# Performance work log

Hardware: AMD Instinct MI355X
Metric: run time of the kernel (lower is better)

Reference implementation:

```python
import jax, jax.numpy as jnp
import numpy as np

D_MODEL = 1024
NUM_HEADS = 16
D_HEAD = D_MODEL // NUM_HEADS  # 64, used only as softmax scale
DFF = 4096
EPS = 1e-6


def _layernorm(x, gamma, beta):
    mu = jnp.mean(x, axis=-1, keepdims=True)
    var = jnp.mean(jnp.square(x - mu), axis=-1, keepdims=True)
    return (x - mu) * jax.lax.rsqrt(var + EPS) * gamma + beta


def _mha(q_in, kv, score, Wq, bq, Wk, bk, Wv, bv, Wo, bo):
    # q_in: [B,Sq,d]; kv: [Sv,d] (broadcast over batch, mirroring unsqueeze(0))
    Q = q_in @ Wq.T + bq                      # [B,Sq,d]
    K = kv @ Wk.T + bk                        # [Sv,d]
    V = kv @ Wv.T + bv                        # [Sv,d]
    scores = (jnp.einsum('bqd,kd->bqk', Q, K) + score) / jnp.sqrt(
        jnp.asarray(D_HEAD, dtype=jnp.float32))
    w = jax.nn.softmax(scores, axis=-1)       # [B,Sq,Sv]
    out = jnp.einsum('bqk,kd->bqd', w, V)     # [B,Sq,d]
    return out @ Wo.T + bo


def setup_inputs() -> dict:
    key = jax.random.key(0)
    ks = jax.random.split(key, 20)
    B, Sq, Sv = 4, 2048, 196
    s = 0.02
    inp = {
        'text_tensor': jax.random.normal(ks[0], (B, Sq, D_MODEL), jnp.float32),
        'visual_tensor': jax.random.normal(ks[1], (Sv, D_MODEL), jnp.float32),
        'score_matrix': jax.random.normal(ks[2], (B, Sq, Sv), jnp.float32),
        'text_tensor2': jax.random.normal(ks[3], (B, Sq, D_MODEL), jnp.float32),
        'visual_tensor2': jax.random.normal(ks[4], (Sv, D_MODEL), jnp.float32),
        'score_matrix2': jax.random.normal(ks[5], (B, Sq, Sv), jnp.float32),
        'Wq': jax.random.normal(ks[6], (D_MODEL, D_MODEL), jnp.float32) * s,
        'bq': jnp.zeros((D_MODEL,), jnp.float32),
        'Wk': jax.random.normal(ks[7], (D_MODEL, D_MODEL), jnp.float32) * s,
        'bk': jnp.zeros((D_MODEL,), jnp.float32),
        'Wv': jax.random.normal(ks[8], (D_MODEL, D_MODEL), jnp.float32) * s,
        'bv': jnp.zeros((D_MODEL,), jnp.float32),
        'Wo': jax.random.normal(ks[9], (D_MODEL, D_MODEL), jnp.float32) * s,
        'bo': jnp.zeros((D_MODEL,), jnp.float32),
        'W1': jax.random.normal(ks[10], (DFF, D_MODEL), jnp.float32) * s,
        'b1': jnp.zeros((DFF,), jnp.float32),
        'W2': jax.random.normal(ks[11], (D_MODEL, DFF), jnp.float32) * s,
        'b2': jnp.zeros((D_MODEL,), jnp.float32),
        'g1': jnp.ones((D_MODEL,), jnp.float32),
        'be1': jnp.zeros((D_MODEL,), jnp.float32),
        'g2': jnp.ones((D_MODEL,), jnp.float32),
        'be2': jnp.zeros((D_MODEL,), jnp.float32),
    }
    return inp


def reference(text_tensor, visual_tensor, score_matrix,
              text_tensor2, visual_tensor2, score_matrix2,
              Wq, bq, Wk, bk, Wv, bv, Wo, bo,
              W1, b1, W2, b2, g1, be1, g2, be2):
    # Branch 1 (dropout is identity in eval mode)
    a1 = _mha(text_tensor, visual_tensor, score_matrix,
              Wq, bq, Wk, bk, Wv, bv, Wo, bo)
    out1 = _layernorm(text_tensor + a1, g1, be1)
    # Branch 2 (shared attention weights, same layernorm1)
    a2 = _mha(text_tensor2, visual_tensor2, score_matrix2,
              Wq, bq, Wk, bk, Wv, bv, Wo, bo)
    out2 = _layernorm(text_tensor2 + a2, g1, be1)
    # Concat along features then MaxPool1d(kernel=2, stride=2) over last dim
    concat = jnp.concatenate([out1, out2], axis=2)       # [B,Sq,2d]
    B, Sq, _ = concat.shape
    pooled = jnp.max(concat.reshape(B, Sq, D_MODEL, 2), axis=-1)  # [B,Sq,d]
    # FFN + residual + layernorm2
    ffn = jax.nn.relu(pooled @ W1.T + b1) @ W2.T + b2
    return _layernorm(pooled + ffn, g2, be2)
```

## Files before the change

kernel.cpp:

```cpp
#include <hip/hip_runtime.h>
#include <hip/hip_bf16.h>
#include <cstdint>
#include <type_traits>

typedef unsigned short u16;
typedef __bf16 bf16x8 __attribute__((ext_vector_type(8)));
typedef float f32x4 __attribute__((ext_vector_type(4)));

#define LN_EPS 1e-6f

enum { BIAS_NONE = 0, BIAS_COL = 1, BIAS_ROW = 2, BIAS_COL2 = 3 };

__device__ __forceinline__ float b2f(u16 h) {
  union { unsigned u; float f; } v;
  v.u = ((unsigned)h) << 16;
  return v.f;
}
__device__ __forceinline__ u16 f2b(float x) {
  return __bfloat16_as_ushort(__float2bfloat16(x));
}

__device__ __forceinline__ void gld_lds16(const void* g, void* l) {
  __builtin_amdgcn_global_load_lds(
      (const __attribute__((address_space(1))) void*)g,
      (__attribute__((address_space(3))) void*)l, 16, 0, 0);
}

__device__ __forceinline__ void st8(float4 a, float4 b, u16* dst) {
  u16 t[8] = {f2b(a.x), f2b(a.y), f2b(a.z), f2b(a.w),
              f2b(b.x), f2b(b.y), f2b(b.z), f2b(b.w)};
  *reinterpret_cast<uint4*>(dst) = *reinterpret_cast<const uint4*>(t);
}

__device__ __forceinline__ void stage8_cvt(const float* src, size_t off,
                                           u16* dst) {
  const float* p = src + off;
  st8(*reinterpret_cast<const float4*>(p),
      *reinterpret_cast<const float4*>(p + 4), dst);
}

template <typename OutT, int BIAS, bool RELU, bool A_RAW, bool B_RAW, int TM,
          int TN, int BK, int NT, int LB>
__global__ __launch_bounds__(NT, LB) void gemm_db(
    const void* __restrict__ A, const void* __restrict__ A2,
    const void* __restrict__ B, const void* __restrict__ B2,
    const float* __restrict__ bias, const float* __restrict__ bias2,
    OutT* __restrict__ C, int M, int N, int K, int lda, int ldb, int MA,
    int NB, int ldc, int Msplit, int rowmask, int colsplit) {
  constexpr int SA = (TM * BK) / (NT * 8);
  constexpr int SB = (TN * BK) / (NT * 8);
  constexpr int AI = (NT == 512) ? 2 : ((TM == 128 && TN == 128) ? 4 : 2);
  constexpr int BJ = (TM == 64 && TN == 64) ? 2 : 4;
  __shared__ __align__(16) u16 As[2][TM * BK];
  __shared__ __align__(16) u16 Bs[2][TN * BK];
  const int tid = threadIdx.x;
  const int lane = tid & 63;
  const int wv = tid >> 6;
  int wr, wc;
  if constexpr (NT == 512) {
    wr = (wv & 3) * 32; wc = (wv >> 2) * 64;
  } else if constexpr (TM == 128 && TN == 128) {
    wr = (wv >> 1) * 64; wc = (wv & 1) * 64;
  } else if constexpr (TM == 128 && TN == 64) {
    wr = wv * 32; wc = 0;
  } else {
    wr = (wv >> 1) * 32; wc = (wv & 1) * 32;
  }
  const int mrow = lane & 15;
  const int quad = lane >> 4;

  int bxi = blockIdx.x, byi = blockIdx.y;
  {
    const int gx = (int)gridDim.x;
    const int nwg = gx * (int)gridDim.y;
    if ((nwg & 7) == 0) {
      int wg = byi * gx + bxi;
      wg = (wg & 7) * (nwg >> 3) + (wg >> 3);
      bxi = wg % gx;
      byi = wg / gx;
    }
  }
  const int bm = byi * TM;
  const int bn = bxi * TN;

  f32x4 acc[AI][BJ];
#pragma unroll
  for (int i = 0; i < AI; i++)
#pragma unroll
    for (int j = 0; j < BJ; j++) acc[i][j] = f32x4{0.f, 0.f, 0.f, 0.f};

  const int e0 = tid * 8;
  const int r0t = e0 >> 5;
  const int swc8 = ((((e0 >> 3) & 3) ^ ((r0t >> 1) & 3)) << 3);

  const void* Asrc[SA];
  size_t aoff[SA];
#pragma unroll
  for (int s = 0; s < SA; s++) {
    const int h = (s * NT * 8) / (TM * 32);
    const int rb = ((s * NT * 8) % (TM * 32)) >> 5;
    int ra = bm + rb + r0t;
    if (ra >= MA) ra = MA - 1;
    Asrc[s] = (ra < Msplit) ? A : A2;
    const int rr = (ra < Msplit) ? ra : ra - Msplit;
    aoff[s] = (size_t)rr * lda + h * 32 + swc8;
  }
  const void* Bb = (bm < Msplit) ? B : B2;
  size_t boff[SB];
#pragma unroll
  for (int s = 0; s < SB; s++) {
    const int h = (s * NT * 8) / (TN * 32);
    const int rb = ((s * NT * 8) % (TN * 32)) >> 5;
    int rbn = bn + rb + r0t;
    if (rbn >= NB) rbn = NB - 1;
    boff[s] = (size_t)rbn * ldb + h * 32 + swc8;
  }

#pragma unroll
  for (int s = 0; s < SA; s++) {
    if constexpr (A_RAW) {
      const float* p = (const float*)Asrc[s] + aoff[s];
      st8(*reinterpret_cast<const float4*>(p),
          *reinterpret_cast<const float4*>(p + 4), &As[0][s * NT * 8 + e0]);
    } else {
      gld_lds16((const u16*)Asrc[s] + aoff[s], &As[0][s * NT * 8 + e0]);
    }
  }
#pragma unroll
  for (int s = 0; s < SB; s++) {
    if constexpr (B_RAW) {
      const float* p = (const float*)Bb + boff[s];
      st8(*reinterpret_cast<const float4*>(p),
          *reinterpret_cast<const float4*>(p + 4), &Bs[0][s * NT * 8 + e0]);
    } else {
      gld_lds16((const u16*)Bb + boff[s], &Bs[0][s * NT * 8 + e0]);
    }
  }
  __syncthreads();

  const int so = ((quad ^ ((mrow >> 1) & 3)) << 3);

  int cur = 0;
  for (int k0 = 0; k0 < K; k0 += BK) {
    const int nk = k0 + BK;
    const bool pf = nk < K;
    float4 fA[SA][2], fB[SB][2];
    if (pf) {
#pragma unroll
      for (int s = 0; s < SA; s++) {
        if constexpr (A_RAW) {
          const float* p = (const float*)Asrc[s] + aoff[s] + nk;
          fA[s][0] = *reinterpret_cast<const float4*>(p);
          fA[s][1] = *reinterpret_cast<const float4*>(p + 4);
        } else {
          gld_lds16((const u16*)Asrc[s] + aoff[s] + nk,
                    &As[cur ^ 1][s * NT * 8 + e0]);
        }
      }
#pragma unroll
      for (int s = 0; s < SB; s++) {
        if constexpr (B_RAW) {
          const float* p = (const float*)Bb + boff[s] + nk;
          fB[s][0] = *reinterpret_cast<const float4*>(p);
          fB[s][1] = *reinterpret_cast<const float4*>(p + 4);
        } else {
          gld_lds16((const u16*)Bb + boff[s] + nk,
                    &Bs[cur ^ 1][s * NT * 8 + e0]);
        }
      }
    }
#pragma unroll
    for (int h = 0; h < BK / 32; h++) {
      bf16x8 af[AI], bfm[BJ];
#pragma unroll
      for (int i = 0; i < AI; i++)
        af[i] = *reinterpret_cast<const bf16x8*>(
            &As[cur][h * TM * 32 + (wr + i * 16 + mrow) * 32 + so]);
#pragma unroll
      for (int j = 0; j < BJ; j++)
        bfm[j] = *reinterpret_cast<const bf16x8*>(
            &Bs[cur][h * TN * 32 + (wc + j * 16 + mrow) * 32 + so]);
#pragma unroll
      for (int i = 0; i < AI; i++)
#pragma unroll
        for (int j = 0; j < BJ; j++)
          acc[i][j] = __builtin_amdgcn_mfma_f32_16x16x32_bf16(
              af[i], bfm[j], acc[i][j], 0, 0, 0);
    }
    if (pf) {
      if constexpr (A_RAW) {
#pragma unroll
        for (int s = 0; s < SA; s++)
          st8(fA[s][0], fA[s][1], &As[cur ^ 1][s * NT * 8 + e0]);
      }
      if constexpr (B_RAW) {
#pragma unroll
        for (int s = 0; s < SB; s++)
          st8(fB[s][0], fB[s][1], &Bs[cur ^ 1][s * NT * 8 + e0]);
      }
    }
    __syncthreads();
    cur ^= 1;
  }

  const float* bp = (bm < Msplit) ? bias : bias2;
#pragma unroll
  for (int i = 0; i < AI; i++) {
#pragma unroll
    for (int j = 0; j < BJ; j++) {
#pragma unroll
      for (int r = 0; r < 4; r++) {
        const int gr = bm + wr + i * 16 + quad * 4 + r;
        const int gc = bn + wc + j * 16 + mrow;
        if (gr < M && gc < N) {
          float v = acc[i][j][r];
          if (BIAS == BIAS_COL) v += bp[gc];
          if (BIAS == BIAS_COL2)
            v += (gc < colsplit) ? bias[gc] : bias2[gc - colsplit];
          if (BIAS == BIAS_ROW) v += bp[gr & rowmask];
          if (RELU) v = fmaxf(v, 0.f);
          if constexpr (std::is_same<OutT, float>::value)
            C[(size_t)gr * ldc + gc] = v;
          else
            C[(size_t)gr * ldc + gc] = f2b(v);
        }
      }
    }
  }
}

__global__ __launch_bounds__(256) void cvt3_k(
    const float* __restrict__ s0, u16* __restrict__ d0,
    const float* __restrict__ s1, u16* __restrict__ d1,
    const float* __restrict__ s2, u16* __restrict__ d2, int blocksPer) {
  const int seg = blockIdx.x / blocksPer;
  const int b = blockIdx.x % blocksPer;
  const float* s = (seg == 0) ? s0 : ((seg == 1) ? s1 : s2);
  u16* d = (seg == 0) ? d0 : ((seg == 1) ? d1 : d2);
  const size_t i = ((size_t)b * 256 + threadIdx.x) * 8;
  stage8_cvt(s, i, d + i);
}

__global__ __launch_bounds__(256) void wqt_k(const float* __restrict__ src,
                                             u16* __restrict__ dst) {
  __shared__ float t[64][65];
  const int bx = blockIdx.x;
  const int by = blockIdx.y;
  const int tx = threadIdx.x & 63;
  const int ty = threadIdx.x >> 6;
#pragma unroll
  for (int i = 0; i < 16; i++)
    t[ty * 16 + i][tx] =
        src[(size_t)(by * 64 + ty * 16 + i) * 1024 + bx * 64 + tx];
  __syncthreads();
#pragma unroll
  for (int i = 0; i < 16; i++)
    dst[(size_t)(bx * 64 + ty * 16 + i) * 1024 + by * 64 + tx] =
        f2b(t[tx][ty * 16 + i]);
}

__global__ __launch_bounds__(256) void kb_k(const u16* __restrict__ Kc,
                                            const float* __restrict__ bq,
                                            float* __restrict__ kb, int ld) {
  const int wvi = blockIdx.x * 4 + (threadIdx.x >> 6);
  const int lane = threadIdx.x & 63;
  const int b = wvi / 224, s = wvi % 224;
  float sum = 0.f;
  if (s < 196) {
    const u16* row = Kc + (size_t)(b * 196 + s) * ld;
    for (int j = lane; j < 1024; j += 64) sum += b2f(row[j]) * bq[j];
  }
#pragma unroll
  for (int off = 32; off > 0; off >>= 1) sum += __shfl_xor(sum, off);
  if (lane == 0) kb[wvi] = sum;
}

__global__ __launch_bounds__(256) void softmax_k(
    u16* __restrict__ Sp, const float* __restrict__ sc1,
    const float* __restrict__ sc2) {
  const int row = blockIdx.x * 4 + (threadIdx.x >> 6);
  const int lane = threadIdx.x & 63;
  const float* score = (row < 8192) ? sc1 + (size_t)row * 196
                                    : sc2 + (size_t)(row - 8192) * 196;
  float x[4];
  float mx = -1e30f;
#pragma unroll
  for (int t = 0; t < 4; t++) {
    const int s = lane + 64 * t;
    float v = -1e30f;
    if (s < 196) v = (b2f(Sp[(size_t)row * 224 + s]) + score[s]) * 0.125f;
    x[t] = v;
    mx = fmaxf(mx, v);
  }
#pragma unroll
  for (int off = 32; off > 0; off >>= 1) mx = fmaxf(mx, __shfl_xor(mx, off));
  float sum = 0.f;
#pragma unroll
  for (int t = 0; t < 4; t++) {
    const int s = lane + 64 * t;
    const float e = (s < 196) ? expf(x[t] - mx) : 0.f;
    x[t] = e;
    sum += e;
  }
#pragma unroll
  for (int off = 32; off > 0; off >>= 1) sum += __shfl_xor(sum, off);
  const float inv = 1.f / sum;
#pragma unroll
  for (int t = 0; t < 4; t++) {
    const int s = lane + 64 * t;
    if (s < 224) Sp[(size_t)row * 224 + s] = f2b((s < 196) ? x[t] * inv : 0.f);
  }
}

__global__ __launch_bounds__(256) void ln_pool_k(
    const float* __restrict__ X1, const float* __restrict__ X2,
    const u16* __restrict__ Y, const float* __restrict__ g,
    const float* __restrict__ be, u16* __restrict__ pooled) {
  const int row16 = blockIdx.x;
  const int br = row16 >> 13;
  const int row = row16 & 8191;
  const int tid = threadIdx.x;
  const int lane = tid & 63;
  const int wv = tid >> 6;
  const float* X = (br ? X2 : X1) + (size_t)row * 1024;
  const u16* Yp = Y + (size_t)row16 * 1024;
  __shared__ float red[4];
  float v[4];
  float s = 0.f;
#pragma unroll
  for (int j = 0; j < 4; j++) {
    const float a = X[tid * 4 + j] + b2f(Yp[tid * 4 + j]);
    v[j] = a;
    s += a;
  }
#pragma unroll
  for (int off = 32; off > 0; off >>= 1) s += __shfl_xor(s, off);
  if (lane == 0) red[wv] = s;
  __syncthreads();
  const float mu = (red[0] + red[1] + red[2] + red[3]) * (1.f / 1024.f);
  __syncthreads();
  float var = 0.f;
#pragma unroll
  for (int j = 0; j < 4; j++) {
    const float d = v[j] - mu;
    var += d * d;
  }
#pragma unroll
  for (int off = 32; off > 0; off >>= 1) var += __shfl_xor(var, off);
  if (lane == 0) red[wv] = var;
  __syncthreads();
  var = (red[0] + red[1] + red[2] + red[3]) * (1.f / 1024.f);
  const float rs = rsqrtf(var + LN_EPS);
  float n[4];
#pragma unroll
  for (int j = 0; j < 4; j++)
    n[j] = (v[j] - mu) * rs * g[tid * 4 + j] + be[tid * 4 + j];
  const size_t pb = (size_t)row * 1024 + br * 512 + tid * 2;
  pooled[pb] = f2b(fmaxf(n[0], n[1]));
  pooled[pb + 1] = f2b(fmaxf(n[2], n[3]));
}

__global__ __launch_bounds__(256) void ln_out_k(
    const u16* __restrict__ X, const u16* __restrict__ Y,
    const float* __restrict__ g, const float* __restrict__ be,
    float* __restrict__ out) {
  const int row = blockIdx.x;
  const int tid = threadIdx.x;
  const int lane = tid & 63;
  const int wv = tid >> 6;
  __shared__ float red[4];
  float v[4];
  float s = 0.f;
  const size_t base = (size_t)row * 1024 + tid * 4;
#pragma unroll
  for (int j = 0; j < 4; j++) {
    const float a = b2f(X[base + j]) + b2f(Y[base + j]);
    v[j] = a;
    s += a;
  }
#pragma unroll
  for (int off = 32; off > 0; off >>= 1) s += __shfl_xor(s, off);
  if (lane == 0) red[wv] = s;
  __syncthreads();
  const float mu = (red[0] + red[1] + red[2] + red[3]) * (1.f / 1024.f);
  __syncthreads();
  float var = 0.f;
#pragma unroll
  for (int j = 0; j < 4; j++) {
    const float d = v[j] - mu;
    var += d * d;
  }
#pragma unroll
  for (int off = 32; off > 0; off >>= 1) var += __shfl_xor(var, off);
  if (lane == 0) red[wv] = var;
  __syncthreads();
  var = (red[0] + red[1] + red[2] + red[3]) * (1.f / 1024.f);
  const float rs = rsqrtf(var + LN_EPS);
#pragma unroll
  for (int j = 0; j < 4; j++)
    out[base + j] = (v[j] - mu) * rs * g[tid * 4 + j] + be[tid * 4 + j];
}

extern "C" void kernel_launch(void* const* d_in, const int* in_sizes, int n_in,
                              void* d_out, int out_size, void* d_ws,
                              size_t ws_size, hipStream_t stream) {
  const size_t MB = 1ull << 20;
  if (ws_size < 61 * MB) return;

  const float* text1 = (const float*)d_in[0];
  const float* vis1 = (const float*)d_in[1];
  const float* sc1 = (const float*)d_in[2];
  const float* text2 = (const float*)d_in[3];
  const float* vis2 = (const float*)d_in[4];
  const float* sc2 = (const float*)d_in[5];
  const float* Wq = (const float*)d_in[6];
  const float* bq = (const float*)d_in[7];
  const float* Wk = (const float*)d_in[8];
  const float* bk = (const float*)d_in[9];
  const float* Wv = (const float*)d_in[10];
  const float* bv = (const float*)d_in[11];
  const float* Wo = (const float*)d_in[12];
  const float* bo = (const float*)d_in[13];
  const float* W1 = (const float*)d_in[14];
  const float* b1 = (const float*)d_in[15];
  const float* W2 = (const float*)d_in[16];
  const float* b2 = (const float*)d_in[17];
  const float* g1 = (const float*)d_in[18];
  const float* be1 = (const float*)d_in[19];
  const float* g2 = (const float*)d_in[20];
  const float* be2 = (const float*)d_in[21];

  const int D = 1024, Sv = 196, SvP = 224, DFF = 4096;
  const int M2 = 16384;
  char* w = (char*)d_ws;
  u16* pooled = (u16*)(w + 0 * MB);
  u16* Wkb = (u16*)(w + 16 * MB);
  u16* Wvb = (u16*)(w + 18 * MB);
  u16* Wob = (u16*)(w + 20 * MB);
  u16* WqT = (u16*)(w + 22 * MB);
  u16* KVcat = (u16*)(w + 24 * MB);
  u16* K2cat = (u16*)(w + 26 * MB);
  u16* VWoT = (u16*)(w + 27 * MB);
  float* kb = (float*)(w + 28 * MB);
  u16* Spcat = (u16*)(w + 29 * MB);
  u16* Ocat = (u16*)d_out;
  u16* H = (u16*)(w + 16 * MB);
  u16* F = (u16*)(w + 48 * MB);
  u16* W1b = (u16*)((char*)d_out + 16 * MB);
  u16* W2b = (u16*)((char*)d_out + 24 * MB);

  auto grid = [](int m, int n, int tm, int tn) {
    return dim3((unsigned)((n + tn - 1) / tn), (unsigned)((m + tm - 1) / tm));
  };

  cvt3_k<<<dim3(3 * 512), 256, 0, stream>>>(Wk, Wkb, Wv, Wvb, Wo, Wob, 512);
  wqt_k<<<dim3(16, 16), 256, 0, stream>>>(Wq, WqT);

  gemm_db<u16, BIAS_COL2, false, true, false, 64, 64, 32, 256, 8>
      <<<grid(2 * Sv, 2 * D, 64, 64), 256, 0, stream>>>(
          vis1, vis2, Wkb, Wkb, bk, bv, KVcat, 2 * Sv, 2 * D, D, D, D, 2 * Sv,
          2 * D, 2 * D, Sv, 0, D);
  gemm_db<u16, BIAS_NONE, false, false, false, 64, 64, 32, 256, 8>
      <<<grid(2 * Sv, D, 64, 64), 256, 0, stream>>>(
          KVcat, KVcat, WqT, WqT, nullptr, nullptr, K2cat, 2 * Sv, D, D, 2 * D,
          D, 2 * Sv, D, D, 2 * Sv, 0, 0);
  kb_k<<<dim3(112), 256, 0, stream>>>(KVcat, bq, kb, 2 * D);
  gemm_db<u16, BIAS_COL, false, true, false, 64, 64, 32, 256, 8>
      <<<grid(M2, Sv, 64, 64), 256, 0, stream>>>(
          text1, text2, K2cat, K2cat + (size_t)Sv * D, kb, kb + SvP, Spcat, M2,
          Sv, D, D, D, M2, Sv, SvP, 8192, 0, 0);
  softmax_k<<<dim3(M2 / 4), 256, 0, stream>>>(Spcat, sc1, sc2);
  gemm_db<u16, BIAS_ROW, false, false, false, 64, 64, 32, 256, 8>
      <<<grid(2 * D, SvP, 64, 64), 256, 0, stream>>>(
          Wob, Wob, KVcat + D, KVcat + (size_t)Sv * 2 * D + D, bo, bo, VWoT,
          2 * D, SvP, D, D, 2 * D, 2 * D, Sv, SvP, D, D - 1, 0);
  gemm_db<u16, BIAS_NONE, false, false, false, 64, 64, 32, 256, 8>
      <<<grid(M2, D, 64, 64), 256, 0, stream>>>(
          Spcat, Spcat + (size_t)8192 * SvP, VWoT, VWoT + (size_t)D * SvP,
          nullptr, nullptr, Ocat, M2, D, SvP, SvP, SvP, M2, D, D, 8192, 0, 0);
  ln_pool_k<<<dim3(M2), 256, 0, stream>>>(text1, text2, Ocat, g1, be1, pooled);

  cvt3_k<<<dim3(2 * 2048), 256, 0, stream>>>(W1, W1b, W2, W2b, W2, W2b, 2048);

  for (int c = 0; c < 2; ++c) {
    const int r0 = c * 4096, rows = 4096;
    gemm_db<u16, BIAS_COL, true, false, false, 128, 128, 32, 256, 5>
        <<<grid(rows, DFF, 128, 128), 256, 0, stream>>>(
            pooled + (size_t)r0 * D, pooled + (size_t)r0 * D, W1b, W1b, b1, b1,
            H, rows, DFF, D, D, D, rows, DFF, DFF, rows, 0, 0);
    gemm_db<u16, BIAS_COL, false, false, false, 64, 64, 64, 256, 5>
        <<<grid(rows, D, 64, 64), 256, 0, stream>>>(
            H, H, W2b, W2b, b2, b2, F, rows, D, DFF, DFF, DFF, rows, D, D,
            rows, 0, 0);
    ln_out_k<<<dim3(rows), 256, 0, stream>>>(
        pooled + (size_t)r0 * D, F, g2, be2, (float*)d_out + (size_t)r0 * D);
  }
}
```

Before: 538.8 us.

## Add specialized 256x256 eight-wave pipelined GEMM for FFN up-projection

Replaces the generic 128x128 tiled GEMM for the first FFN layer (4096x4096x1024, bias+ReLU) with a hardcoded 256x256 tile kernel using 8 waves, split-K-half LDS buffers with XOR swizzle, direct global-to-LDS loads interleaved into eight phases per K pair, and setprio around MFMA bursts. Block indices are remapped for L2 locality. The larger tile raises arithmetic intensity and the finer-grained phase scheduling is meant to overlap loads with MFMA; the cost is heavy register and LDS use (occupancy 2 blocks) and a kernel hardwired to these exact dimensions.

```diff
diff --git a/kernel.cpp b/kernel.cpp
--- a/kernel.cpp
+++ b/kernel.cpp
@@ -37,6 +37,121 @@
   const float* p = src + off;
   st8(*reinterpret_cast<const float4*>(p),
       *reinterpret_cast<const float4*>(p + 4), dst);
+}
+
+#define PH8(BUF, KS, FH, VM, ...)                                           \
+  do {                                                                      \
+    asm volatile("s_waitcnt vmcnt(" #VM ")" ::: "memory");                  \
+    __builtin_amdgcn_sched_barrier(0);                                      \
+    __builtin_amdgcn_s_barrier();                                           \
+    __builtin_amdgcn_sched_barrier(0);                                      \
+    bf16x8 af[4], bfr[4];                                                   \
+    _Pragma("unroll") for (int j = 0; j < 4; j++) {                         \
+      const int ra = wm * 128 + ((FH) * 4 + j) * 16 + mrow;                 \
+      af[j] = *reinterpret_cast<const bf16x8*>(                             \
+          &As[BUF][KS][ra * 32 + ((quad ^ ((ra >> 1) & 3)) << 3)]);         \
+    }                                                                       \
+    _Pragma("unroll") for (int j = 0; j < 4; j++) {                         \
+      const int rb = wn * 64 + j * 16 + mrow;                               \
+      bfr[j] = *reinterpret_cast<const bf16x8*>(                            \
+          &Bs[BUF][KS][rb * 32 + ((quad ^ ((rb >> 1) & 3)) << 3)]);         \
+    }                                                                       \
+    __VA_ARGS__;                                                            \
+    __builtin_amdgcn_s_setprio(1);                                          \
+    _Pragma("unroll") for (int j = 0; j < 4; j++)                           \
+        _Pragma("unroll") for (int c = 0; c < 4; c++) acc[(FH) * 4 + j][c] = \
+            __builtin_amdgcn_mfma_f32_16x16x32_bf16(                        \
+                af[j], bfr[c], acc[(FH) * 4 + j][c], 0, 0, 0);              \
+    __builtin_amdgcn_s_setprio(0);                                          \
+  } while (0)
+
+__global__ __launch_bounds__(512, 2) void gemm_8p(
+    const u16* __restrict__ A, const u16* __restrict__ B,
+    const float* __restrict__ bias, u16* __restrict__ C) {
+  __shared__ __align__(16) u16 As[2][2][256 * 32];
+  __shared__ __align__(16) u16 Bs[2][2][256 * 32];
+  const int tid = threadIdx.x;
+  const int lane = tid & 63;
+  const int wid = tid >> 6;
+  const int wm = wid >> 2;
+  const int wn = wid & 3;
+  const int mrow = lane & 15;
+  const int quad = lane >> 4;
+  int bxi = blockIdx.x, byi = blockIdx.y;
+  {
+    int wg = byi * 16 + bxi;
+    wg = (wg & 7) * 32 + (wg >> 3);
+    bxi = wg & 15;
+    byi = wg >> 4;
+  }
+  const int bm = byi * 256;
+  const int bn = bxi * 256;
+
+  const int i0 = tid;
+  const int i1 = 512 + tid;
+  const int r0 = i0 >> 2, c0s = (((i0 & 3) ^ ((r0 >> 1) & 3)) << 3);
+  const int r1 = i1 >> 2, c1s = (((i1 & 3) ^ ((r1 >> 1) & 3)) << 3);
+  const size_t oa0 = (size_t)(bm + r0) * 1024 + c0s;
+  const size_t oa1 = (size_t)(bm + r1) * 1024 + c1s;
+  const size_t ob0 = (size_t)(bn + r0) * 1024 + c0s;
+  const size_t ob1 = (size_t)(bn + r1) * 1024 + c1s;
+
+#define STG_A(T, KH)                                                       \
+  do {                                                                     \
+    gld_lds16(A + oa0 + (T) * 64 + (KH) * 32, &As[(T) & 1][KH][i0 * 8]);   \
+    gld_lds16(A + oa1 + (T) * 64 + (KH) * 32, &As[(T) & 1][KH][i1 * 8]);   \
+  } while (0)
+#define STG_B(T, KH)                                                       \
+  do {                                                                     \
+    gld_lds16(B + ob0 + (T) * 64 + (KH) * 32, &Bs[(T) & 1][KH][i0 * 8]);   \
+    gld_lds16(B + ob1 + (T) * 64 + (KH) * 32, &Bs[(T) & 1][KH][i1 * 8]);   \
+  } while (0)
+
+  f32x4 acc[8][4];
+#pragma unroll
+  for (int i = 0; i < 8; i++)
+#pragma unroll
+    for (int j = 0; j < 4; j++) acc[i][j] = f32x4{0.f, 0.f, 0.f, 0.f};
+
+  STG_A(0, 0); STG_B(0, 0); STG_A(0, 1); STG_B(0, 1);
+  STG_A(1, 0); STG_B(1, 0);
+
+#pragma unroll 1
+  for (int t = 0; t < 14; t += 2) {
+    PH8(0, 0, 0, 8, STG_A(t + 1, 1));
+    PH8(0, 0, 1, 8, STG_B(t + 1, 1));
+    PH8(0, 1, 0, 8, STG_A(t + 2, 0));
+    PH8(0, 1, 1, 8, STG_B(t + 2, 0));
+    PH8(1, 0, 0, 8, STG_A(t + 2, 1));
+    PH8(1, 0, 1, 8, STG_B(t + 2, 1));
+    PH8(1, 1, 0, 8, STG_A(t + 3, 0));
+    PH8(1, 1, 1, 8, STG_B(t + 3, 0));
+  }
+  PH8(0, 0, 0, 8, STG_A(15, 1));
+  PH8(0, 0, 1, 8, STG_B(15, 1));
+  PH8(0, 1, 0, 8, (void)0);
+  PH8(0, 1, 1, 8, (void)0);
+  PH8(1, 0, 0, 4, (void)0);
+  PH8(1, 0, 1, 4, (void)0);
+  PH8(1, 1, 0, 0, (void)0);
+  PH8(1, 1, 1, 0, (void)0);
+
+#pragma unroll
+  for (int fr = 0; fr < 8; fr++) {
+#pragma unroll
+    for (int fc = 0; fc < 4; fc++) {
+#pragma unroll
+      for (int r = 0; r < 4; r++) {
+        const int gr = bm + wm * 128 + fr * 16 + quad * 4 + r;
+        const int gc = bn + wn * 64 + fc * 16 + mrow;
+        float v = acc[fr][fc][r] + bias[gc];
+        v = fmaxf(v, 0.f);
+        C[(size_t)gr * 4096 + gc] = f2b(v);
+      }
+    }
+  }
+#undef STG_A
+#undef STG_B
 }
 
 template <typename OutT, int BIAS, bool RELU, bool A_RAW, bool B_RAW, int TM,
@@ -484,10 +599,8 @@
 
   for (int c = 0; c < 2; ++c) {
     const int r0 = c * 4096, rows = 4096;
-    gemm_db<u16, BIAS_COL, true, false, false, 128, 128, 32, 256, 5>
-        <<<grid(rows, DFF, 128, 128), 256, 0, stream>>>(
-            pooled + (size_t)r0 * D, pooled + (size_t)r0 * D, W1b, W1b, b1, b1,
-            H, rows, DFF, D, D, D, rows, DFF, DFF, rows, 0, 0);
+    gemm_8p<<<dim3(16, 16), 512, 0, stream>>>(pooled + (size_t)r0 * D, W1b,
+                                              b1, H);
     gemm_db<u16, BIAS_COL, false, false, false, 64, 64, 64, 256, 5>
         <<<grid(rows, D, 64, 64), 256, 0, stream>>>(
             H, H, W2b, W2b, b2, b2, F, rows, D, DFF, DFF, DFF, rows, D, D,
```

Measured after the change: 521.7 us. -3.2%, faster.
